# Kernel tuning notes

Hardware: AMD Instinct MI355X
Metric: run time of the kernel (lower is better)

The kernel has to match this reference:

```python
import jax, jax.numpy as jnp
import numpy as np

B, D_IN, D_Z, D_H, D_T, D_REC = 8192, 1024, 256, 256, 16, 256


def _softplus_beta(x, beta):
    # torch F.softplus(x, beta) = (1/beta) * log(1 + exp(beta*x))
    return jax.nn.softplus(beta * x) / beta


def setup_inputs() -> dict:
    key = jax.random.key(0)
    ks = jax.random.split(key, 17)
    w = lambda k, o, i: jax.random.normal(k, (o, i), jnp.float32) * (1.0 / np.sqrt(i))
    return {
        "I_t": jax.random.uniform(ks[0], (B, D_IN), jnp.float32),
        "h_m_1": jax.random.uniform(ks[1], (B, D_H), jnp.float32),
        "z_m_1": jax.random.uniform(ks[2], (B, D_Z), jnp.float32),
        "theta_m_1": jax.random.normal(ks[3], (B, D_T), jnp.float32),
        "eps_z": jax.random.normal(ks[4], (B, D_Z), jnp.float32),
        "eps_zhat": jax.random.normal(ks[5], (B, D_Z), jnp.float32),
        "W_post_mu": w(ks[6], D_Z, D_IN),
        "W_post_lv": w(ks[7], D_Z, D_IN),
        "W_z2h": w(ks[8], D_H, D_Z),
        "W_h2h": w(ks[9], D_H, D_H),
        "W_prior_mu": w(ks[10], D_Z, D_H),
        "W_prior_lv": w(ks[11], D_Z, D_H),
        "W_i2t": w(ks[12], D_T, D_IN),
        "W_vip2t": w(ks[13], D_T, D_Z),
        "W_t2z": w(ks[14], D_Z, D_T),
        "W_rec1": w(ks[15], D_REC, D_Z),
        "W_rec2": w(ks[16], D_IN, D_REC),
    }


def reference(I_t, h_m_1, z_m_1, theta_m_1, eps_z, eps_zhat,
              W_post_mu, W_post_lv, W_z2h, W_h2h, W_prior_mu, W_prior_lv,
              W_i2t, W_vip2t, W_t2z, W_rec1, W_rec2):
    relu = jax.nn.relu
    # prior pathway (perception_only=True branch)
    mu_p = relu(h_m_1 @ W_prior_mu.T)                       # [B, D_Z]
    sigma_p = _softplus_beta(h_m_1 @ W_prior_lv.T, 1.2)     # [B, D_Z]
    # theta dynamics; vip_to_theta has Positive parametrization -> relu(W)
    theta_h = (0.5 * theta_m_1 + 0.1 * (I_t @ W_i2t.T)
               - jax.lax.stop_gradient(sigma_p) @ relu(W_vip2t).T)  # [B, D_T]
    theta = 0.001 * _softplus_beta(theta_h, 0.5)
    # posterior + reparameterized sample
    mu_q = relu(I_t @ W_post_mu.T)
    sigma_q = relu(I_t @ W_post_lv.T)
    raw_z = jnp.clip(mu_q + eps_z * sigma_q, 0.0, 1.0)
    thresholds = 10.0 * (theta @ relu(W_t2z).T)             # Positive parametrization
    z = relu(raw_z - thresholds)                            # [B, D_Z]
    # reconstruction (two bias-free linears + sigmoid)
    I_hat = jax.nn.sigmoid((z @ W_rec1.T) @ W_rec2.T)       # [B, D_IN]
    # higher-state update and prior sample
    h = relu(z_m_1 @ W_z2h.T + h_m_1 @ W_h2h.T)             # [B, D_H]
    z_hat = mu_p + eps_zhat * sigma_p                       # [B, D_Z]
    # losses (as in torch forward)
    spatial = jnp.mean((I_t - I_hat) ** 2)
    temporal = jnp.mean((jax.lax.stop_gradient(z) - z_hat) ** 2)
    energy = jnp.mean(jnp.abs(z))
    return (I_hat, z, h, z_hat, spatial, temporal, energy)
```

## Files before the change

kernel.cpp:

```cpp
#include <hip/hip_runtime.h>
#include <math.h>

#define BB 8192
#define DIN 1024
#define DZ 256
#define DH 256
#define DT 16
#define DREC 256

#define OFF_IHAT 0
#define OFF_Z    (BB * DIN)
#define OFF_H    (OFF_Z + BB * DZ)
#define OFF_ZHAT (OFF_H + BB * DH)
#define OFF_SCAL (OFF_ZHAT + BB * DZ)

#define WS_HBF   0
#define WS_ZM1   2097152
#define WS_W     4194304
#define W_PM  (WS_W + 0)
#define W_PL  (W_PM + 262144)
#define W_Z2H (W_PL + 262144)
#define W_H2H (W_Z2H + 65536)
#define W_PRM (W_H2H + 65536)
#define W_PRL (W_PRM + 65536)
#define W_I2T (W_PRL + 65536)
#define W_VIP (W_I2T + 16384)
#define W_R1  (W_VIP + 4096)
#define W_R2  (W_R1 + 65536)
#define WS_ENDW  (W_R2 + 262144)
#define WS_SIGMA WS_ENDW
#define WS_ZBF   (WS_SIGMA + 2097152)
#define WS_R1BF  (WS_ZBF + 2097152)

typedef unsigned short u16;
typedef __attribute__((ext_vector_type(8))) unsigned short u16x8;
typedef __attribute__((ext_vector_type(8))) __bf16 bf16x8;
typedef __attribute__((ext_vector_type(4))) float f32x4;

#define MFMA __builtin_amdgcn_mfma_f32_16x16x32_bf16

__device__ inline u16 f2bf(float f) {
  unsigned u = __builtin_bit_cast(unsigned, f);
  u += 0x7fff + ((u >> 16) & 1);
  return (u16)(u >> 16);
}
__device__ inline float softplus_stable(float y) {
  return (y > 20.f) ? y : log1pf(expf(y));
}
__device__ inline bf16x8 gf(const u16* p) {
  return __builtin_bit_cast(bf16x8, *(const u16x8*)p);
}
__device__ inline f32x4 fzero() { return (f32x4){0.f, 0.f, 0.f, 0.f}; }

__device__ inline float block_sum256(float v, float* rbuf) {
#pragma unroll
  for (int off = 32; off > 0; off >>= 1) v += __shfl_down(v, off, 64);
  __syncthreads();
  if ((threadIdx.x & 63) == 0) rbuf[threadIdx.x >> 6] = v;
  __syncthreads();
  return rbuf[0] + rbuf[1] + rbuf[2] + rbuf[3];
}
__device__ inline float block_sum512(float v, float* rbuf) {
#pragma unroll
  for (int off = 32; off > 0; off >>= 1) v += __shfl_down(v, off, 64);
  __syncthreads();
  if ((threadIdx.x & 63) == 0) rbuf[threadIdx.x >> 6] = v;
  __syncthreads();
  float s = 0.f;
#pragma unroll
  for (int i = 0; i < 8; ++i) s += rbuf[i];
  return s;
}

__device__ inline void decode4(int id, int rows, int& row0, int& col0) {
  int xcd = id & 7, t = id >> 3;
  col0 = (t & 3) * 64;
  row0 = ((t >> 2) * 8 + xcd) * rows;
}

__device__ inline void dmaA32(u16* tile, const u16* __restrict__ gsrc,
                              int row0, int ldk, int k0) {
  const int lane = threadIdx.x & 63, w = threadIdx.x >> 6;
  int rb = w * 8;
  int r = rb + (lane >> 3);
  int gl = (lane & 7) ^ (r & 7);
  const u16* src = gsrc + (size_t)(row0 + r) * ldk + k0 + gl * 8;
  u16* dst = tile + rb * 64;
  __builtin_amdgcn_global_load_lds(
      (const __attribute__((address_space(1))) unsigned int*)(const void*)src,
      (__attribute__((address_space(3))) unsigned int*)(void*)dst, 16, 0, 0);
}
__device__ inline void dmaB64(u16* tile, const u16* __restrict__ gsrc,
                              int row0, int ldk, int k0) {
  const int lane = threadIdx.x & 63, w = threadIdx.x >> 6;
#pragma unroll
  for (int c = 0; c < 2; ++c) {
    int rb = w * 16 + c * 8;
    int r = rb + (lane >> 3);
    int gl = (lane & 7) ^ (r & 7);
    const u16* src = gsrc + (size_t)(row0 + r) * ldk + k0 + gl * 8;
    u16* dst = tile + rb * 64;
    __builtin_amdgcn_global_load_lds(
        (const __attribute__((address_space(1))) unsigned int*)(const void*)src,
        (__attribute__((address_space(3))) unsigned int*)(void*)dst, 16, 0, 0);
  }
}
__device__ inline bf16x8 rd(const u16* tile, int r, int gl) {
  return gf(tile + r * 64 + ((gl ^ (r & 7)) * 8));
}

__device__ inline void stg64x256(u16* tile, const u16* __restrict__ g,
                                 int row0, int ldk, int k0) {
  const int lane = threadIdx.x & 63, w = threadIdx.x >> 6;
#pragma unroll
  for (int i = 0; i < 4; ++i) {
    int rb = (w * 4 + i) * 2;
    int r = rb + (lane >> 5);
    int d = lane & 31;
    int s = d ^ (r & 7);
    const u16* src = g + (size_t)(row0 + r) * ldk + k0 + s * 8;
    u16* dst = tile + rb * 256;
    __builtin_amdgcn_global_load_lds(
        (const __attribute__((address_space(1))) unsigned int*)(const void*)src,
        (__attribute__((address_space(3))) unsigned int*)(void*)dst, 16, 0, 0);
  }
}
__device__ inline void stg16x256(u16* tile, const u16* __restrict__ g,
                                 int ldk, int k0) {
  const int lane = threadIdx.x & 63, w = threadIdx.x >> 6;
  int rb = w * 2;
  int r = rb + (lane >> 5);
  int d = lane & 31;
  int s = d ^ (r & 7);
  const u16* src = g + (size_t)r * ldk + k0 + s * 8;
  u16* dst = tile + rb * 256;
  __builtin_amdgcn_global_load_lds(
      (const __attribute__((address_space(1))) unsigned int*)(const void*)src,
      (__attribute__((address_space(3))) unsigned int*)(void*)dst, 16, 0, 0);
}
__device__ inline bf16x8 rd256(const u16* tile, int r, int j) {
  return gf(tile + r * 256 + ((j ^ (r & 7)) * 8));
}

__global__ __launch_bounds__(256) void k_cvt(
    const float* __restrict__ I_t, const float* __restrict__ h_m_1,
    const float* __restrict__ z_m_1, const float* __restrict__ Wpm,
    const float* __restrict__ Wpl, const float* __restrict__ Wz2h,
    const float* __restrict__ Wh2h, const float* __restrict__ Wprm,
    const float* __restrict__ Wprl, const float* __restrict__ Wi2t,
    const float* __restrict__ Wv, const float* __restrict__ Wr1,
    const float* __restrict__ Wr2, u16* __restrict__ dstI,
    u16* __restrict__ dstW) {
  const int S1 = 8388608, S2 = 10485760, S3 = 12582912, S4 = 12845056,
            S5 = 13107200, S6 = 13172736, S7 = 13238272, S8 = 13303808,
            S9 = 13369344, S10 = 13385728, S11 = 13389824, S12 = 13455360,
            S13 = 13717504;
  int nchunk = S13 / 8;
  for (int c = blockIdx.x * 256 + threadIdx.x; c < nchunk;
       c += gridDim.x * 256) {
    int f = c * 8;
    const float* src;
    float scale = 1.f;
    bool nrelu = false;
    u16* dst;
    if (f < S1) {
      src = I_t + f;
      dst = dstI + f;
    } else {
      dst = dstW + (f - S1);
      if (f < S2)       src = h_m_1 + (f - S1);
      else if (f < S3)  src = z_m_1 + (f - S2);
      else if (f < S4)  src = Wpm + (f - S3);
      else if (f < S5)  src = Wpl + (f - S4);
      else if (f < S6)  src = Wz2h + (f - S5);
      else if (f < S7)  src = Wh2h + (f - S6);
      else if (f < S8)  src = Wprm + (f - S7);
      else if (f < S9)  src = Wprl + (f - S8);
      else if (f < S10) { src = Wi2t + (f - S9);  scale = 0.1f; }
      else if (f < S11) { src = Wv + (f - S10);   nrelu = true; }
      else if (f < S12) src = Wr1 + (f - S11);
      else              src = Wr2 + (f - S12);
    }
    float4 v0 = *(const float4*)(src);
    float4 v1 = *(const float4*)(src + 4);
    float vals[8] = {v0.x, v0.y, v0.z, v0.w, v1.x, v1.y, v1.z, v1.w};
    u16x8 o;
#pragma unroll
    for (int j = 0; j < 8; ++j) {
      float x = vals[j];
      x = nrelu ? -fmaxf(x, 0.f) : x * scale;
      o[j] = f2bf(x);
    }
    *(u16x8*)(dst) = o;
  }
}

__global__ __launch_bounds__(256, 4) void k_hp(
    const u16* __restrict__ h_bf, const u16* __restrict__ zm1,
    const u16* __restrict__ Wh2h, const u16* __restrict__ Wprm,
    const u16* __restrict__ Wprl, const u16* __restrict__ Wz2h,
    const float* __restrict__ eps_zhat, float* __restrict__ h_out,
    float* __restrict__ zhat_out, u16* __restrict__ sigma_bf) {
  __shared__ __align__(16) u16 smem[2048 + 3 * 4096];
  u16* As = smem;
  u16* B0s = smem + 2048;
  u16* B1s = B0s + 4096;
  u16* B2s = B1s + 4096;
  const int tid = threadIdx.x, lane = tid & 63, w = tid >> 6;
  const int frow = lane & 15, fq = lane >> 4;
  const int wr = w & 1, wc = w >> 1;
  int row0, col0;
  decode4(blockIdx.x, 32, row0, col0);

  f32x4 ah[2], am[2], as_[2];
#pragma unroll
  for (int i = 0; i < 2; ++i) { ah[i] = fzero(); am[i] = fzero(); as_[i] = fzero(); }

  for (int k0 = 0; k0 < DH; k0 += 64) {
    __syncthreads();
    dmaA32(As, h_bf, row0, DH, k0);
    dmaB64(B0s, Wh2h, col0, DH, k0);
    dmaB64(B1s, Wprm, col0, DH, k0);
    dmaB64(B2s, Wprl, col0, DH, k0);
    __syncthreads();
#pragma unroll
    for (int ks = 0; ks < 2; ++ks) {
      bf16x8 a = rd(As, wr * 16 + frow, ks * 4 + fq);
#pragma unroll
      for (int ni = 0; ni < 2; ++ni) {
        int br = wc * 32 + ni * 16 + frow;
        ah[ni]  = MFMA(a, rd(B0s, br, ks * 4 + fq), ah[ni], 0, 0, 0);
        am[ni]  = MFMA(a, rd(B1s, br, ks * 4 + fq), am[ni], 0, 0, 0);
        as_[ni] = MFMA(a, rd(B2s, br, ks * 4 + fq), as_[ni], 0, 0, 0);
      }
    }
  }
  for (int k0 = 0; k0 < DZ; k0 += 64) {
    __syncthreads();
    dmaA32(As, zm1, row0, DZ, k0);
    dmaB64(B0s, Wz2h, col0, DZ, k0);
    __syncthreads();
#pragma unroll
    for (int ks = 0; ks < 2; ++ks) {
      bf16x8 a = rd(As, wr * 16 + frow, ks * 4 + fq);
#pragma unroll
      for (int ni = 0; ni < 2; ++ni)
        ah[ni] = MFMA(a, rd(B0s, wc * 32 + ni * 16 + frow, ks * 4 + fq),
                      ah[ni], 0, 0, 0);
    }
  }
  __syncthreads();
  float* ht = (float*)smem;
  float* mt = (float*)(smem + 4224);
  float* st = (float*)(smem + 8448);
#pragma unroll
  for (int ni = 0; ni < 2; ++ni)
#pragma unroll
    for (int r = 0; r < 4; ++r) {
      int lr = wr * 16 + fq * 4 + r;
      int ln = wc * 32 + ni * 16 + frow;
      ht[lr * 66 + ln] = fmaxf(ah[ni][r], 0.f);
      mt[lr * 66 + ln] = fmaxf(am[ni][r], 0.f);
      st[lr * 66 + ln] = softplus_stable(1.2f * as_[ni][r]) * (1.f / 1.2f);
    }
  __syncthreads();
  {
    int lr2 = tid >> 3, c0 = (tid & 7) * 8;
    int m2 = row0 + lr2;
    float h8[8], mu8[8], sg8[8];
#pragma unroll
    for (int j = 0; j < 8; ++j) {
      h8[j] = ht[lr2 * 66 + c0 + j];
      mu8[j] = mt[lr2 * 66 + c0 + j];
      sg8[j] = st[lr2 * 66 + c0 + j];
    }
    float* hp = h_out + (size_t)m2 * DH + col0 + c0;
    *(float4*)hp = make_float4(h8[0], h8[1], h8[2], h8[3]);
    *(float4*)(hp + 4) = make_float4(h8[4], h8[5], h8[6], h8[7]);
    const float* ep = eps_zhat + (size_t)m2 * DZ + col0 + c0;
    float4 e0 = ((const float4*)ep)[0], e1 = ((const float4*)ep)[1];
    float e8[8] = {e0.x, e0.y, e0.z, e0.w, e1.x, e1.y, e1.z, e1.w};
    float zh8[8];
    u16x8 sb;
#pragma unroll
    for (int j = 0; j < 8; ++j) {
      zh8[j] = mu8[j] + e8[j] * sg8[j];
      sb[j] = f2bf(sg8[j]);
    }
    float* zp = zhat_out + (size_t)m2 * DZ + col0 + c0;
    *(float4*)zp = make_float4(zh8[0], zh8[1], zh8[2], zh8[3]);
    *(float4*)(zp + 4) = make_float4(zh8[4], zh8[5], zh8[6], zh8[7]);
    *(u16x8*)(sigma_bf + (size_t)m2 * DZ + col0 + c0) = sb;
  }
}

__global__ __launch_bounds__(512, 2) void k_post(
    const u16* __restrict__ I_bf, const u16* __restrict__ Wpm,
    const u16* __restrict__ Wpl, const u16* __restrict__ Wi2t,
    const u16* __restrict__ Wv, const u16* __restrict__ sigma_bf,
    const float* __restrict__ theta_m_1, const float* __restrict__ W_t2z,
    const float* __restrict__ eps_z, const float* __restrict__ zhat,
    float* __restrict__ z_out, u16* __restrict__ z_bf,
    float* __restrict__ scal) {
  __shared__ __align__(16) u16 smem[36864];
  __shared__ float thwt[128 * 17 + 64 * 17];
  __shared__ float rbuf[8];
  const int tid = threadIdx.x, lane = tid & 63, w = tid >> 6;
  const int frow = lane & 15, fq = lane >> 4;
  int row0, col0;
  {
    int xcd = blockIdx.x & 7, t = blockIdx.x >> 3;
    col0 = (t & 3) * 64;
    row0 = ((t >> 2) * 8 + xcd) * 128;
  }
  u16* b0 = smem;

  f32x4 mu[4], sg[4], tt = fzero();
#pragma unroll
  for (int i = 0; i < 4; ++i) { mu[i] = fzero(); sg[i] = fzero(); }

  const u16* Abase = I_bf + (size_t)(row0 + w * 16 + frow) * DIN;
  const u16* Sbase = sigma_bf + (size_t)(row0 + w * 16 + frow) * DZ;
  bf16x8 ar[8];

#pragma unroll 1
  for (int p = 0; p < 4; ++p) {
    int kwin = p * 256;
    stg64x256(b0, Wpm, col0, DIN, kwin);
    stg64x256(b0 + 16384, Wpl, col0, DIN, kwin);
    stg16x256(b0 + 32768, Wi2t, DIN, kwin);
#pragma unroll
    for (int kk = 0; kk < 8; ++kk)
      ar[kk] = gf(Abase + kwin + kk * 32 + fq * 8);
    __syncthreads();
#pragma unroll
    for (int kk = 0; kk < 8; ++kk) {
#pragma unroll
      for (int n = 0; n < 4; ++n) {
        mu[n] = MFMA(ar[kk], rd256(b0, n * 16 + frow, kk * 4 + fq),
                     mu[n], 0, 0, 0);
        sg[n] = MFMA(ar[kk], rd256(b0 + 16384, n * 16 + frow, kk * 4 + fq),
                     sg[n], 0, 0, 0);
      }
      tt = MFMA(ar[kk], rd256(b0 + 32768, frow, kk * 4 + fq), tt, 0, 0, 0);
    }
    __syncthreads();
  }
  stg16x256(b0 + 32768, Wv, DZ, 0);
#pragma unroll
  for (int kk = 0; kk < 8; ++kk) ar[kk] = gf(Sbase + kk * 32 + fq * 8);
  __syncthreads();
#pragma unroll
  for (int kk = 0; kk < 8; ++kk)
    tt = MFMA(ar[kk], rd256(b0 + 32768, frow, kk * 4 + fq), tt, 0, 0, 0);
  __syncthreads();

  float* mt   = (float*)smem;
  float* st   = (float*)(smem + 16896);
  float* th_s = thwt;
  float* wt_s = thwt + 128 * 17;

#pragma unroll
  for (int r = 0; r < 4; ++r) {
    int lr = w * 16 + fq * 4 + r;
    float th = 0.5f * theta_m_1[(size_t)(row0 + lr) * DT + frow] + tt[r];
    th_s[lr * 17 + frow] = 0.002f * softplus_stable(0.5f * th);
  }
  for (int idx = tid; idx < 64 * 16; idx += 512) {
    int n = idx >> 4, j = idx & 15;
    wt_s[n * 17 + j] = 10.f * fmaxf(W_t2z[(col0 + n) * DT + j], 0.f);
  }
#pragma unroll
  for (int n = 0; n < 4; ++n)
#pragma unroll
    for (int r = 0; r < 4; ++r) {
      int lr = w * 16 + fq * 4 + r;
      int ln = n * 16 + frow;
      mt[lr * 66 + ln] = fmaxf(mu[n][r], 0.f);
      st[lr * 66 + ln] = fmaxf(sg[n][r], 0.f);
    }
  __syncthreads();
  float tsum = 0.f, esum = 0.f;
  {
    int lr2 = tid >> 2, c0 = (tid & 3) * 16;
    int m2 = row0 + lr2;
    float thv[16];
#pragma unroll
    for (int j = 0; j < 16; ++j) thv[j] = th_s[lr2 * 17 + j];
#pragma unroll
    for (int gb = 0; gb < 2; ++gb) {
      int c = c0 + gb * 8;
      float mu8[8], sg8[8];
#pragma unroll
      for (int j = 0; j < 8; ++j) {
        mu8[j] = mt[lr2 * 66 + c + j];
        sg8[j] = st[lr2 * 66 + c + j];
      }
      const float* ep = eps_z + (size_t)m2 * DZ + col0 + c;
      float4 e0 = ((const float4*)ep)[0], e1 = ((const float4*)ep)[1];
      float e8[8] = {e0.x, e0.y, e0.z, e0.w, e1.x, e1.y, e1.z, e1.w};
      float z8[8];
#pragma unroll
      for (int j = 0; j < 8; ++j) {
        float raw = mu8[j] + e8[j] * sg8[j];
        raw = fminf(fmaxf(raw, 0.f), 1.f);
        float thr = 0.f;
#pragma unroll
        for (int jj = 0; jj < 16; ++jj)
          thr = fmaf(thv[jj], wt_s[(c + j) * 17 + jj], thr);
        z8[j] = fmaxf(raw - thr, 0.f);
      }
      float* zp = z_out + (size_t)m2 * DZ + col0 + c;
      *(float4*)zp = make_float4(z8[0], z8[1], z8[2], z8[3]);
      *(float4*)(zp + 4) = make_float4(z8[4], z8[5], z8[6], z8[7]);
      u16x8 zb;
#pragma unroll
      for (int j = 0; j < 8; ++j) zb[j] = f2bf(z8[j]);
      *(u16x8*)(z_bf + (size_t)m2 * DZ + col0 + c) = zb;
      const float* zhp = zhat + (size_t)m2 * DZ + col0 + c;
      float4 h0 = ((const float4*)zhp)[0], h1 = ((const float4*)zhp)[1];
      float zh8[8] = {h0.x, h0.y, h0.z, h0.w, h1.x, h1.y, h1.z, h1.w};
#pragma unroll
      for (int j = 0; j < 8; ++j) {
        float d = z8[j] - zh8[j];
        tsum += d * d;
        esum += z8[j];
      }
    }
  }
  float t = block_sum512(tsum, rbuf);
  if (tid == 0) atomicAdd(scal + 1, t * (1.f / ((float)BB * DZ)));
  float e = block_sum512(esum, rbuf);
  if (tid == 0) atomicAdd(scal + 2, e * (1.f / ((float)BB * DZ)));
}

__global__ __launch_bounds__(256, 4) void k_rec1(const u16* __restrict__ z_bf,
                                                 const u16* __restrict__ Wr1,
                                                 u16* __restrict__ r1_bf) {
  __shared__ __align__(16) u16 smem[2048 + 4096];
  u16* As = smem;
  u16* B0s = smem + 2048;
  const int tid = threadIdx.x, lane = tid & 63, w = tid >> 6;
  const int frow = lane & 15, fq = lane >> 4;
  const int wr = w & 1, wc = w >> 1;
  int row0, col0;
  decode4(blockIdx.x, 32, row0, col0);
  f32x4 acc[2] = {fzero(), fzero()};
  for (int k0 = 0; k0 < DZ; k0 += 64) {
    __syncthreads();
    dmaA32(As, z_bf, row0, DZ, k0);
    dmaB64(B0s, Wr1, col0, DZ, k0);
    __syncthreads();
#pragma unroll
    for (int ks = 0; ks < 2; ++ks) {
      bf16x8 a = rd(As, wr * 16 + frow, ks * 4 + fq);
#pragma unroll
      for (int ni = 0; ni < 2; ++ni)
        acc[ni] = MFMA(a, rd(B0s, wc * 32 + ni * 16 + frow, ks * 4 + fq),
                       acc[ni], 0, 0, 0);
    }
  }
  __syncthreads();
  float* rt = (float*)smem;
#pragma unroll
  for (int ni = 0; ni < 2; ++ni)
#pragma unroll
    for (int r = 0; r < 4; ++r) {
      int lr = wr * 16 + fq * 4 + r;
      int ln = wc * 32 + ni * 16 + frow;
      rt[lr * 66 + ln] = acc[ni][r];
    }
  __syncthreads();
  {
    int lr2 = tid >> 3, c0 = (tid & 7) * 8;
    int m2 = row0 + lr2;
    u16x8 rb;
#pragma unroll
    for (int j = 0; j < 8; ++j) rb[j] = f2bf(rt[lr2 * 66 + c0 + j]);
    *(u16x8*)(r1_bf + (size_t)m2 * DREC + col0 + c0) = rb;
  }
}

__global__ __launch_bounds__(256, 4) void k_rec2(const u16* __restrict__ r1_bf,
                                                 const u16* __restrict__ Wr2,
                                                 const float* __restrict__ I_t,
                                                 float* __restrict__ ihat_out,
                                                 float* __restrict__ scal) {
  __shared__ __align__(16) u16 smem[4096 + 4096];
  u16* As = smem;
  u16* B0s = smem + 4096;
  __shared__ float rbuf[4];
  const int tid = threadIdx.x, lane = tid & 63, w = tid >> 6;
  const int frow = lane & 15, fq = lane >> 4;
  int row0, col0;
  {
    int id = blockIdx.x;
    int xcd = id & 7, t = id >> 3;
    col0 = (t & 15) * 64;
    row0 = ((t >> 4) * 8 + xcd) * 64;
  }
  f32x4 acc[4] = {fzero(), fzero(), fzero(), fzero()};
  for (int k0 = 0; k0 < DREC; k0 += 64) {
    __syncthreads();
    dmaB64(As, r1_bf, row0, DREC, k0);
    dmaB64(B0s, Wr2, col0, DREC, k0);
    __syncthreads();
#pragma unroll
    for (int ks = 0; ks < 2; ++ks) {
      bf16x8 a = rd(As, w * 16 + frow, ks * 4 + fq);
#pragma unroll
      for (int ni = 0; ni < 4; ++ni)
        acc[ni] = MFMA(a, rd(B0s, ni * 16 + frow, ks * 4 + fq), acc[ni], 0, 0, 0);
    }
  }
  float lsum = 0.f;
  float* it = (float*)smem;
#pragma unroll 1
  for (int p = 0; p < 2; ++p) {
    __syncthreads();
    if ((w >> 1) == p) {
#pragma unroll
      for (int ni = 0; ni < 4; ++ni)
#pragma unroll
        for (int r = 0; r < 4; ++r) {
          int lrl = (w & 1) * 16 + fq * 4 + r;
          int ln = ni * 16 + frow;
          it[lrl * 66 + ln] = 1.f / (1.f + expf(-acc[ni][r]));
        }
    }
    __syncthreads();
    int lr2 = tid >> 3, c0 = (tid & 7) * 8;
    int m2 = row0 + p * 32 + lr2;
    float i8[8];
#pragma unroll
    for (int j = 0; j < 8; ++j) i8[j] = it[lr2 * 66 + c0 + j];
    float* op = ihat_out + (size_t)m2 * DIN + col0 + c0;
    *(float4*)op = make_float4(i8[0], i8[1], i8[2], i8[3]);
    *(float4*)(op + 4) = make_float4(i8[4], i8[5], i8[6], i8[7]);
    const float* ip = I_t + (size_t)m2 * DIN + col0 + c0;
    float4 a0 = ((const float4*)ip)[0], a1 = ((const float4*)ip)[1];
    float t8[8] = {a0.x, a0.y, a0.z, a0.w, a1.x, a1.y, a1.z, a1.w};
#pragma unroll
    for (int j = 0; j < 8; ++j) {
      float d = t8[j] - i8[j];
      lsum += d * d;
    }
  }
  float s = block_sum256(lsum, rbuf);
  if (tid == 0) atomicAdd(scal + 0, s * (1.f / ((float)BB * DIN)));
}

extern "C" void kernel_launch(void* const* d_in, const int* in_sizes, int n_in,
                              void* d_out, int out_size, void* d_ws,
                              size_t ws_size, hipStream_t stream) {
  const float* I_t       = (const float*)d_in[0];
  const float* h_m_1     = (const float*)d_in[1];
  const float* z_m_1     = (const float*)d_in[2];
  const float* theta_m_1 = (const float*)d_in[3];
  const float* eps_z     = (const float*)d_in[4];
  const float* eps_zhat  = (const float*)d_in[5];
  const float* W_post_mu = (const float*)d_in[6];
  const float* W_post_lv = (const float*)d_in[7];
  const float* W_z2h     = (const float*)d_in[8];
  const float* W_h2h     = (const float*)d_in[9];
  const float* W_prior_mu= (const float*)d_in[10];
  const float* W_prior_lv= (const float*)d_in[11];
  const float* W_i2t     = (const float*)d_in[12];
  const float* W_vip2t   = (const float*)d_in[13];
  const float* W_t2z     = (const float*)d_in[14];
  const float* W_rec1    = (const float*)d_in[15];
  const float* W_rec2    = (const float*)d_in[16];

  float* out = (float*)d_out;
  float* ihat = out + OFF_IHAT;
  float* zout = out + OFF_Z;
  float* hout = out + OFF_H;
  float* zhat = out + OFF_ZHAT;
  float* scal = out + OFF_SCAL;

  u16* ws_u = (u16*)d_ws;
  u16* I_bf = (u16*)ihat;
  u16* h_bf = ws_u + WS_HBF;
  u16* zm1_bf = ws_u + WS_ZM1;
  u16* sigma_bf = ws_u + WS_SIGMA;
  u16* z_bf = ws_u + WS_ZBF;
  u16* r1_bf = ws_u + WS_R1BF;

  hipMemsetAsync(scal, 0, 3 * sizeof(float), stream);

  k_cvt<<<2048, 256, 0, stream>>>(I_t, h_m_1, z_m_1, W_post_mu, W_post_lv,
                                  W_z2h, W_h2h, W_prior_mu, W_prior_lv, W_i2t,
                                  W_vip2t, W_rec1, W_rec2, I_bf, ws_u + WS_HBF);

  k_hp<<<1024, 256, 0, stream>>>(h_bf, zm1_bf, ws_u + W_H2H, ws_u + W_PRM,
                                 ws_u + W_PRL, ws_u + W_Z2H, eps_zhat, hout,
                                 zhat, sigma_bf);
  k_post<<<256, 512, 0, stream>>>(I_bf, ws_u + W_PM, ws_u + W_PL,
                                  ws_u + W_I2T, ws_u + W_VIP, sigma_bf,
                                  theta_m_1, W_t2z, eps_z, zhat, zout, z_bf,
                                  scal);
  k_rec1<<<1024, 256, 0, stream>>>(z_bf, ws_u + W_R1, r1_bf);
  k_rec2<<<2048, 256, 0, stream>>>(r1_bf, ws_u + W_R2, I_t, ihat, scal);
}
```

Baseline: 238.3 us.

## Double-buffer LDS staging in hp, post, rec1 and rec2 GEMM kernels

Converts the K-loops of the four GEMM kernels to double-buffered shared memory. The next K slice is issued with global_load_lds while the current slice is consumed, so each step needs one barrier instead of two. The posterior kernel drops from 256-wide K windows to 128-wide windows across two alternating buffers, prefetching A fragments into alternating register sets in a fully unrolled sequence. The point is to overlap global-to-LDS transfer with MFMA work. The cost is twice the LDS per block, a lower occupancy hint for k_hp (4 to 2 blocks), and more registers for the prefetched A fragments.

```diff
diff --git a/kernel.cpp b/kernel.cpp
--- a/kernel.cpp
+++ b/kernel.cpp
@@ -109,37 +109,64 @@
   return gf(tile + r * 64 + ((gl ^ (r & 7)) * 8));
 }
 
-__device__ inline void stg64x256(u16* tile, const u16* __restrict__ g,
+__device__ inline void stg64x128(u16* tile, const u16* __restrict__ g,
                                  int row0, int ldk, int k0) {
   const int lane = threadIdx.x & 63, w = threadIdx.x >> 6;
 #pragma unroll
-  for (int i = 0; i < 4; ++i) {
-    int rb = (w * 4 + i) * 2;
-    int r = rb + (lane >> 5);
-    int d = lane & 31;
+  for (int i = 0; i < 2; ++i) {
+    int rb = (w * 2 + i) * 4;
+    int r = rb + (lane >> 4);
+    int d = lane & 15;
     int s = d ^ (r & 7);
     const u16* src = g + (size_t)(row0 + r) * ldk + k0 + s * 8;
-    u16* dst = tile + rb * 256;
+    u16* dst = tile + rb * 128;
     __builtin_amdgcn_global_load_lds(
         (const __attribute__((address_space(1))) unsigned int*)(const void*)src,
         (__attribute__((address_space(3))) unsigned int*)(void*)dst, 16, 0, 0);
   }
 }
-__device__ inline void stg16x256(u16* tile, const u16* __restrict__ g,
+__device__ inline void stg16x128(u16* tile, const u16* __restrict__ g,
                                  int ldk, int k0) {
   const int lane = threadIdx.x & 63, w = threadIdx.x >> 6;
-  int rb = w * 2;
-  int r = rb + (lane >> 5);
-  int d = lane & 31;
-  int s = d ^ (r & 7);
-  const u16* src = g + (size_t)r * ldk + k0 + s * 8;
-  u16* dst = tile + rb * 256;
-  __builtin_amdgcn_global_load_lds(
-      (const __attribute__((address_space(1))) unsigned int*)(const void*)src,
-      (__attribute__((address_space(3))) unsigned int*)(void*)dst, 16, 0, 0);
-}
-__device__ inline bf16x8 rd256(const u16* tile, int r, int j) {
-  return gf(tile + r * 256 + ((j ^ (r & 7)) * 8));
+  if (w < 4) {
+    int rb = w * 4;
+    int r = rb + (lane >> 4);
+    int d = lane & 15;
+    int s = d ^ (r & 7);
+    const u16* src = g + (size_t)r * ldk + k0 + s * 8;
+    u16* dst = tile + rb * 128;
+    __builtin_amdgcn_global_load_lds(
+        (const __attribute__((address_space(1))) unsigned int*)(const void*)src,
+        (__attribute__((address_space(3))) unsigned int*)(void*)dst, 16, 0, 0);
+  }
+}
+__device__ inline bf16x8 rd128(const u16* tile, int r, int j) {
+  return gf(tile + r * 128 + ((j ^ (r & 7)) * 8));
+}
+
+__device__ inline void lda4(bf16x8 (&ar)[4], const u16* base, int kwin,
+                            int fq) {
+#pragma unroll
+  for (int kk = 0; kk < 4; ++kk) ar[kk] = gf(base + kwin + kk * 32 + fq * 8);
+}
+__device__ inline void cmpMain(const u16* buf, bf16x8 (&ar)[4], f32x4 (&mu)[4],
+                               f32x4 (&sg)[4], f32x4& tt, int frow, int fq) {
+#pragma unroll
+  for (int kk = 0; kk < 4; ++kk) {
+    int j = kk * 4 + fq;
+#pragma unroll
+    for (int n = 0; n < 4; ++n) {
+      mu[n] = MFMA(ar[kk], rd128(buf, n * 16 + frow, j), mu[n], 0, 0, 0);
+      sg[n] = MFMA(ar[kk], rd128(buf + 8192, n * 16 + frow, j), sg[n], 0, 0, 0);
+    }
+    tt = MFMA(ar[kk], rd128(buf + 16384, frow, j), tt, 0, 0, 0);
+  }
+}
+__device__ inline void cmpSig(const u16* buf, bf16x8 (&ar)[4], f32x4& tt,
+                              int frow, int fq) {
+#pragma unroll
+  for (int kk = 0; kk < 4; ++kk)
+    tt = MFMA(ar[kk], rd128(buf + 16384, frow, kk * 4 + fq), tt, 0, 0, 0);
 }
 
 __global__ __launch_bounds__(256) void k_cvt(
@@ -195,17 +222,13 @@
   }
 }
 
-__global__ __launch_bounds__(256, 4) void k_hp(
+__global__ __launch_bounds__(256, 2) void k_hp(
     const u16* __restrict__ h_bf, const u16* __restrict__ zm1,
     const u16* __restrict__ Wh2h, const u16* __restrict__ Wprm,
     const u16* __restrict__ Wprl, const u16* __restrict__ Wz2h,
     const float* __restrict__ eps_zhat, float* __restrict__ h_out,
     float* __restrict__ zhat_out, u16* __restrict__ sigma_bf) {
-  __shared__ __align__(16) u16 smem[2048 + 3 * 4096];
-  u16* As = smem;
-  u16* B0s = smem + 2048;
-  u16* B1s = B0s + 4096;
-  u16* B2s = B1s + 4096;
+  __shared__ __align__(16) u16 smem[2 * 14336];
   const int tid = threadIdx.x, lane = tid & 63, w = tid >> 6;
   const int frow = lane & 15, fq = lane >> 4;
   const int wr = w & 1, wc = w >> 1;
@@ -216,37 +239,55 @@
 #pragma unroll
   for (int i = 0; i < 2; ++i) { ah[i] = fzero(); am[i] = fzero(); as_[i] = fzero(); }
 
-  for (int k0 = 0; k0 < DH; k0 += 64) {
+  dmaA32(smem, h_bf, row0, DH, 0);
+  dmaB64(smem + 2048, Wh2h, col0, DH, 0);
+  dmaB64(smem + 6144, Wprm, col0, DH, 0);
+  dmaB64(smem + 10240, Wprl, col0, DH, 0);
+
+#pragma unroll 1
+  for (int t = 0; t < 8; ++t) {
     __syncthreads();
-    dmaA32(As, h_bf, row0, DH, k0);
-    dmaB64(B0s, Wh2h, col0, DH, k0);
-    dmaB64(B1s, Wprm, col0, DH, k0);
-    dmaB64(B2s, Wprl, col0, DH, k0);
-    __syncthreads();
-#pragma unroll
-    for (int ks = 0; ks < 2; ++ks) {
-      bf16x8 a = rd(As, wr * 16 + frow, ks * 4 + fq);
-#pragma unroll
-      for (int ni = 0; ni < 2; ++ni) {
-        int br = wc * 32 + ni * 16 + frow;
-        ah[ni]  = MFMA(a, rd(B0s, br, ks * 4 + fq), ah[ni], 0, 0, 0);
-        am[ni]  = MFMA(a, rd(B1s, br, ks * 4 + fq), am[ni], 0, 0, 0);
-        as_[ni] = MFMA(a, rd(B2s, br, ks * 4 + fq), as_[ni], 0, 0, 0);
+    u16* cs = smem + (t & 1) * 14336;
+    u16* ns = smem + ((t + 1) & 1) * 14336;
+    if (t < 7) {
+      int u = t + 1;
+      if (u < 4) {
+        int k0 = u * 64;
+        dmaA32(ns, h_bf, row0, DH, k0);
+        dmaB64(ns + 2048, Wh2h, col0, DH, k0);
+        dmaB64(ns + 6144, Wprm, col0, DH, k0);
+        dmaB64(ns + 10240, Wprl, col0, DH, k0);
+      } else {
+        int k0 = (u - 4) * 64;
+        dmaA32(ns, zm1, row0, DZ, k0);
+        dmaB64(ns + 2048, Wz2h, col0, DZ, k0);
       }
     }
-  }
-  for (int k0 = 0; k0 < DZ; k0 += 64) {
-    __syncthreads();
-    dmaA32(As, zm1, row0, DZ, k0);
-    dmaB64(B0s, Wz2h, col0, DZ, k0);
-    __syncthreads();
-#pragma unroll
-    for (int ks = 0; ks < 2; ++ks) {
-      bf16x8 a = rd(As, wr * 16 + frow, ks * 4 + fq);
-#pragma unroll
-      for (int ni = 0; ni < 2; ++ni)
-        ah[ni] = MFMA(a, rd(B0s, wc * 32 + ni * 16 + frow, ks * 4 + fq),
-                      ah[ni], 0, 0, 0);
+    const u16* As = cs;
+    const u16* B0s = cs + 2048;
+    if (t < 4) {
+      const u16* B1s = cs + 6144;
+      const u16* B2s = cs + 10240;
+#pragma unroll
+      for (int ks = 0; ks < 2; ++ks) {
+        bf16x8 a = rd(As, wr * 16 + frow, ks * 4 + fq);
+#pragma unroll
+        for (int ni = 0; ni < 2; ++ni) {
+          int br = wc * 32 + ni * 16 + frow;
+          ah[ni]  = MFMA(a, rd(B0s, br, ks * 4 + fq), ah[ni], 0, 0, 0);
+          am[ni]  = MFMA(a, rd(B1s, br, ks * 4 + fq), am[ni], 0, 0, 0);
+          as_[ni] = MFMA(a, rd(B2s, br, ks * 4 + fq), as_[ni], 0, 0, 0);
+        }
+      }
+    } else {
+#pragma unroll
+      for (int ks = 0; ks < 2; ++ks) {
+        bf16x8 a = rd(As, wr * 16 + frow, ks * 4 + fq);
+#pragma unroll
+        for (int ni = 0; ni < 2; ++ni)
+          ah[ni] = MFMA(a, rd(B0s, wc * 32 + ni * 16 + frow, ks * 4 + fq),
+                        ah[ni], 0, 0, 0);
+      }
     }
   }
   __syncthreads();
@@ -302,7 +343,7 @@
     const float* __restrict__ eps_z, const float* __restrict__ zhat,
     float* __restrict__ z_out, u16* __restrict__ z_bf,
     float* __restrict__ scal) {
-  __shared__ __align__(16) u16 smem[36864];
+  __shared__ __align__(16) u16 smem[2 * 18432];
   __shared__ float thwt[128 * 17 + 64 * 17];
   __shared__ float rbuf[8];
   const int tid = threadIdx.x, lane = tid & 63, w = tid >> 6;
@@ -314,6 +355,7 @@
     row0 = ((t >> 2) * 8 + xcd) * 128;
   }
   u16* b0 = smem;
+  u16* b1 = smem + 18432;
 
   f32x4 mu[4], sg[4], tt = fzero();
 #pragma unroll
@@ -321,40 +363,38 @@
 
   const u16* Abase = I_bf + (size_t)(row0 + w * 16 + frow) * DIN;
   const u16* Sbase = sigma_bf + (size_t)(row0 + w * 16 + frow) * DZ;
-  bf16x8 ar[8];
-
-#pragma unroll 1
-  for (int p = 0; p < 4; ++p) {
-    int kwin = p * 256;
-    stg64x256(b0, Wpm, col0, DIN, kwin);
-    stg64x256(b0 + 16384, Wpl, col0, DIN, kwin);
-    stg16x256(b0 + 32768, Wi2t, DIN, kwin);
-#pragma unroll
-    for (int kk = 0; kk < 8; ++kk)
-      ar[kk] = gf(Abase + kwin + kk * 32 + fq * 8);
-    __syncthreads();
-#pragma unroll
-    for (int kk = 0; kk < 8; ++kk) {
-#pragma unroll
-      for (int n = 0; n < 4; ++n) {
-        mu[n] = MFMA(ar[kk], rd256(b0, n * 16 + frow, kk * 4 + fq),
-                     mu[n], 0, 0, 0);
-        sg[n] = MFMA(ar[kk], rd256(b0 + 16384, n * 16 + frow, kk * 4 + fq),
-                     sg[n], 0, 0, 0);
-      }
-      tt = MFMA(ar[kk], rd256(b0 + 32768, frow, kk * 4 + fq), tt, 0, 0, 0);
-    }
-    __syncthreads();
-  }
-  stg16x256(b0 + 32768, Wv, DZ, 0);
-#pragma unroll
-  for (int kk = 0; kk < 8; ++kk) ar[kk] = gf(Sbase + kk * 32 + fq * 8);
-  __syncthreads();
-#pragma unroll
-  for (int kk = 0; kk < 8; ++kk)
-    tt = MFMA(ar[kk], rd256(b0 + 32768, frow, kk * 4 + fq), tt, 0, 0, 0);
-  __syncthreads();
-
+  bf16x8 arA[4], arB[4];
+
+#define STGM(buf, k0)                        \
+  stg64x128(buf, Wpm, col0, DIN, k0);        \
+  stg64x128((buf) + 8192, Wpl, col0, DIN, k0);\
+  stg16x128((buf) + 16384, Wi2t, DIN, k0)
+
+  STGM(b0, 0);
+  lda4(arA, Abase, 0, fq);
+  __syncthreads(); STGM(b1, 128); lda4(arB, Abase, 128, fq);
+  cmpMain(b0, arA, mu, sg, tt, frow, fq);
+  __syncthreads(); STGM(b0, 256); lda4(arA, Abase, 256, fq);
+  cmpMain(b1, arB, mu, sg, tt, frow, fq);
+  __syncthreads(); STGM(b1, 384); lda4(arB, Abase, 384, fq);
+  cmpMain(b0, arA, mu, sg, tt, frow, fq);
+  __syncthreads(); STGM(b0, 512); lda4(arA, Abase, 512, fq);
+  cmpMain(b1, arB, mu, sg, tt, frow, fq);
+  __syncthreads(); STGM(b1, 640); lda4(arB, Abase, 640, fq);
+  cmpMain(b0, arA, mu, sg, tt, frow, fq);
+  __syncthreads(); STGM(b0, 768); lda4(arA, Abase, 768, fq);
+  cmpMain(b1, arB, mu, sg, tt, frow, fq);
+  __syncthreads(); STGM(b1, 896); lda4(arB, Abase, 896, fq);
+  cmpMain(b0, arA, mu, sg, tt, frow, fq);
+  __syncthreads(); stg16x128(b0 + 16384, Wv, DZ, 0); lda4(arA, Sbase, 0, fq);
+  cmpMain(b1, arB, mu, sg, tt, frow, fq);
+  __syncthreads(); stg16x128(b1 + 16384, Wv, DZ, 128); lda4(arB, Sbase, 128, fq);
+  cmpSig(b0, arA, tt, frow, fq);
+  __syncthreads();
+  cmpSig(b1, arB, tt, frow, fq);
+#undef STGM
+
+  __syncthreads();
   float* mt   = (float*)smem;
   float* st   = (float*)(smem + 16896);
   float* th_s = thwt;
@@ -437,26 +477,32 @@
 __global__ __launch_bounds__(256, 4) void k_rec1(const u16* __restrict__ z_bf,
                                                  const u16* __restrict__ Wr1,
                                                  u16* __restrict__ r1_bf) {
-  __shared__ __align__(16) u16 smem[2048 + 4096];
-  u16* As = smem;
-  u16* B0s = smem + 2048;
+  __shared__ __align__(16) u16 smem[2 * 6144];
   const int tid = threadIdx.x, lane = tid & 63, w = tid >> 6;
   const int frow = lane & 15, fq = lane >> 4;
   const int wr = w & 1, wc = w >> 1;
   int row0, col0;
   decode4(blockIdx.x, 32, row0, col0);
   f32x4 acc[2] = {fzero(), fzero()};
-  for (int k0 = 0; k0 < DZ; k0 += 64) {
+
+  dmaA32(smem, z_bf, row0, DZ, 0);
+  dmaB64(smem + 2048, Wr1, col0, DZ, 0);
+#pragma unroll 1
+  for (int t = 0; t < 4; ++t) {
     __syncthreads();
-    dmaA32(As, z_bf, row0, DZ, k0);
-    dmaB64(B0s, Wr1, col0, DZ, k0);
-    __syncthreads();
+    u16* cs = smem + (t & 1) * 6144;
+    u16* ns = smem + ((t + 1) & 1) * 6144;
+    if (t < 3) {
+      int k0 = (t + 1) * 64;
+      dmaA32(ns, z_bf, row0, DZ, k0);
+      dmaB64(ns + 2048, Wr1, col0, DZ, k0);
+    }
 #pragma unroll
     for (int ks = 0; ks < 2; ++ks) {
-      bf16x8 a = rd(As, wr * 16 + frow, ks * 4 + fq);
+      bf16x8 a = rd(cs, wr * 16 + frow, ks * 4 + fq);
 #pragma unroll
       for (int ni = 0; ni < 2; ++ni)
-        acc[ni] = MFMA(a, rd(B0s, wc * 32 + ni * 16 + frow, ks * 4 + fq),
+        acc[ni] = MFMA(a, rd(cs + 2048, wc * 32 + ni * 16 + frow, ks * 4 + fq),
                        acc[ni], 0, 0, 0);
     }
   }
@@ -486,9 +532,7 @@
                                                  const float* __restrict__ I_t,
                                                  float* __restrict__ ihat_out,
                                                  float* __restrict__ scal) {
-  __shared__ __align__(16) u16 smem[4096 + 4096];
-  u16* As = smem;
-  u16* B0s = smem + 4096;
+  __shared__ __align__(16) u16 smem[2 * 8192];
   __shared__ float rbuf[4];
   const int tid = threadIdx.x, lane = tid & 63, w = tid >> 6;
   const int frow = lane & 15, fq = lane >> 4;
@@ -500,17 +544,26 @@
     row0 = ((t >> 4) * 8 + xcd) * 64;
   }
   f32x4 acc[4] = {fzero(), fzero(), fzero(), fzero()};
-  for (int k0 = 0; k0 < DREC; k0 += 64) {
+
+  dmaB64(smem, r1_bf, row0, DREC, 0);
+  dmaB64(smem + 4096, Wr2, col0, DREC, 0);
+#pragma unroll 1
+  for (int t = 0; t < 4; ++t) {
     __syncthreads();
-    dmaB64(As, r1_bf, row0, DREC, k0);
-    dmaB64(B0s, Wr2, col0, DREC, k0);
-    __syncthreads();
+    u16* cs = smem + (t & 1) * 8192;
+    u16* ns = smem + ((t + 1) & 1) * 8192;
+    if (t < 3) {
+      int k0 = (t + 1) * 64;
+      dmaB64(ns, r1_bf, row0, DREC, k0);
+      dmaB64(ns + 4096, Wr2, col0, DREC, k0);
+    }
 #pragma unroll
     for (int ks = 0; ks < 2; ++ks) {
-      bf16x8 a = rd(As, w * 16 + frow, ks * 4 + fq);
+      bf16x8 a = rd(cs, w * 16 + frow, ks * 4 + fq);
 #pragma unroll
       for (int ni = 0; ni < 4; ++ni)
-        acc[ni] = MFMA(a, rd(B0s, ni * 16 + frow, ks * 4 + fq), acc[ni], 0, 0, 0);
+        acc[ni] = MFMA(a, rd(cs + 4096, ni * 16 + frow, ks * 4 + fq),
+                       acc[ni], 0, 0, 0);
     }
   }
   float lsum = 0.f;
```

New measurement: 236.3 us. Within noise of the previous version (-0.8%).

## Double-buffer k_post weight staging and give each wave two row tiles

Applied to the files above, without the earlier changes.

Rewrites the posterior kernel to use 256 threads, with each wave handling 32 rows (two MFMA row tiles) so every LDS B-fragment read is reused twice. K windows shrink to 128 and alternate between two LDS buffers, so the next window's global-to-LDS DMA and A-register loads overlap MFMA work on the current one. The aim is to hide load latency and cut LDS read traffic. In exchange, register pressure per thread doubles and fewer waves are resident, since launch bounds drop to 256 threads with min 1 block.

```diff
diff --git a/kernel.cpp b/kernel.cpp
--- a/kernel.cpp
+++ b/kernel.cpp
@@ -60,17 +60,6 @@
   __syncthreads();
   return rbuf[0] + rbuf[1] + rbuf[2] + rbuf[3];
 }
-__device__ inline float block_sum512(float v, float* rbuf) {
-#pragma unroll
-  for (int off = 32; off > 0; off >>= 1) v += __shfl_down(v, off, 64);
-  __syncthreads();
-  if ((threadIdx.x & 63) == 0) rbuf[threadIdx.x >> 6] = v;
-  __syncthreads();
-  float s = 0.f;
-#pragma unroll
-  for (int i = 0; i < 8; ++i) s += rbuf[i];
-  return s;
-}
 
 __device__ inline void decode4(int id, int rows, int& row0, int& col0) {
   int xcd = id & 7, t = id >> 3;
@@ -109,37 +98,75 @@
   return gf(tile + r * 64 + ((gl ^ (r & 7)) * 8));
 }
 
-__device__ inline void stg64x256(u16* tile, const u16* __restrict__ g,
-                                 int row0, int ldk, int k0) {
+__device__ inline void stg64q(u16* tile, const u16* __restrict__ g,
+                              int row0, int ldk, int k0) {
   const int lane = threadIdx.x & 63, w = threadIdx.x >> 6;
 #pragma unroll
   for (int i = 0; i < 4; ++i) {
-    int rb = (w * 4 + i) * 2;
-    int r = rb + (lane >> 5);
-    int d = lane & 31;
+    int rb = w * 16 + i * 4;
+    int r = rb + (lane >> 4);
+    int d = lane & 15;
     int s = d ^ (r & 7);
     const u16* src = g + (size_t)(row0 + r) * ldk + k0 + s * 8;
-    u16* dst = tile + rb * 256;
+    u16* dst = tile + rb * 128;
     __builtin_amdgcn_global_load_lds(
         (const __attribute__((address_space(1))) unsigned int*)(const void*)src,
         (__attribute__((address_space(3))) unsigned int*)(void*)dst, 16, 0, 0);
   }
 }
-__device__ inline void stg16x256(u16* tile, const u16* __restrict__ g,
-                                 int ldk, int k0) {
+__device__ inline void stg16q(u16* tile, const u16* __restrict__ g,
+                              int ldk, int k0) {
   const int lane = threadIdx.x & 63, w = threadIdx.x >> 6;
-  int rb = w * 2;
-  int r = rb + (lane >> 5);
-  int d = lane & 31;
+  int rb = w * 4;
+  int r = rb + (lane >> 4);
+  int d = lane & 15;
   int s = d ^ (r & 7);
   const u16* src = g + (size_t)r * ldk + k0 + s * 8;
-  u16* dst = tile + rb * 256;
+  u16* dst = tile + rb * 128;
   __builtin_amdgcn_global_load_lds(
       (const __attribute__((address_space(1))) unsigned int*)(const void*)src,
       (__attribute__((address_space(3))) unsigned int*)(void*)dst, 16, 0, 0);
 }
-__device__ inline bf16x8 rd256(const u16* tile, int r, int j) {
-  return gf(tile + r * 256 + ((j ^ (r & 7)) * 8));
+__device__ inline bf16x8 rd128(const u16* tile, int r, int j) {
+  return gf(tile + r * 128 + ((j ^ (r & 7)) * 8));
+}
+
+__device__ inline void lda8(bf16x8 (&ar)[2][4], const u16* a0, const u16* a1,
+                            int kwin, int fq) {
+#pragma unroll
+  for (int kk = 0; kk < 4; ++kk) {
+    ar[0][kk] = gf(a0 + kwin + kk * 32 + fq * 8);
+    ar[1][kk] = gf(a1 + kwin + kk * 32 + fq * 8);
+  }
+}
+__device__ inline void cmpMain2(const u16* buf, bf16x8 (&ar)[2][4],
+                                f32x4 (&mu)[2][4], f32x4 (&sg)[2][4],
+                                f32x4 (&tt)[2], int frow, int fq) {
+#pragma unroll
+  for (int kk = 0; kk < 4; ++kk) {
+    int j = kk * 4 + fq;
+#pragma unroll
+    for (int n = 0; n < 4; ++n) {
+      bf16x8 bm = rd128(buf, n * 16 + frow, j);
+      mu[0][n] = MFMA(ar[0][kk], bm, mu[0][n], 0, 0, 0);
+      mu[1][n] = MFMA(ar[1][kk], bm, mu[1][n], 0, 0, 0);
+      bf16x8 bs = rd128(buf + 8192, n * 16 + frow, j);
+      sg[0][n] = MFMA(ar[0][kk], bs, sg[0][n], 0, 0, 0);
+      sg[1][n] = MFMA(ar[1][kk], bs, sg[1][n], 0, 0, 0);
+    }
+    bf16x8 bt = rd128(buf + 16384, frow, j);
+    tt[0] = MFMA(ar[0][kk], bt, tt[0], 0, 0, 0);
+    tt[1] = MFMA(ar[1][kk], bt, tt[1], 0, 0, 0);
+  }
+}
+__device__ inline void cmpSig2(const u16* buf, bf16x8 (&ar)[2][4],
+                               f32x4 (&tt)[2], int frow, int fq) {
+#pragma unroll
+  for (int kk = 0; kk < 4; ++kk) {
+    bf16x8 bt = rd128(buf + 16384, frow, kk * 4 + fq);
+    tt[0] = MFMA(ar[0][kk], bt, tt[0], 0, 0, 0);
+    tt[1] = MFMA(ar[1][kk], bt, tt[1], 0, 0, 0);
+  }
 }
 
 __global__ __launch_bounds__(256) void k_cvt(
@@ -294,7 +321,7 @@
   }
 }
 
-__global__ __launch_bounds__(512, 2) void k_post(
+__global__ __launch_bounds__(256, 1) void k_post(
     const u16* __restrict__ I_bf, const u16* __restrict__ Wpm,
     const u16* __restrict__ Wpl, const u16* __restrict__ Wi2t,
     const u16* __restrict__ Wv, const u16* __restrict__ sigma_bf,
@@ -302,9 +329,9 @@
     const float* __restrict__ eps_z, const float* __restrict__ zhat,
     float* __restrict__ z_out, u16* __restrict__ z_bf,
     float* __restrict__ scal) {
-  __shared__ __align__(16) u16 smem[36864];
+  __shared__ __align__(16) u16 smem[2 * 18432];
   __shared__ float thwt[128 * 17 + 64 * 17];
-  __shared__ float rbuf[8];
+  __shared__ float rbuf[4];
   const int tid = threadIdx.x, lane = tid & 63, w = tid >> 6;
   const int frow = lane & 15, fq = lane >> 4;
   int row0, col0;
@@ -314,81 +341,91 @@
     row0 = ((t >> 2) * 8 + xcd) * 128;
   }
   u16* b0 = smem;
-
-  f32x4 mu[4], sg[4], tt = fzero();
-#pragma unroll
-  for (int i = 0; i < 4; ++i) { mu[i] = fzero(); sg[i] = fzero(); }
-
-  const u16* Abase = I_bf + (size_t)(row0 + w * 16 + frow) * DIN;
-  const u16* Sbase = sigma_bf + (size_t)(row0 + w * 16 + frow) * DZ;
-  bf16x8 ar[8];
-
-#pragma unroll 1
-  for (int p = 0; p < 4; ++p) {
-    int kwin = p * 256;
-    stg64x256(b0, Wpm, col0, DIN, kwin);
-    stg64x256(b0 + 16384, Wpl, col0, DIN, kwin);
-    stg16x256(b0 + 32768, Wi2t, DIN, kwin);
-#pragma unroll
-    for (int kk = 0; kk < 8; ++kk)
-      ar[kk] = gf(Abase + kwin + kk * 32 + fq * 8);
-    __syncthreads();
-#pragma unroll
-    for (int kk = 0; kk < 8; ++kk) {
-#pragma unroll
-      for (int n = 0; n < 4; ++n) {
-        mu[n] = MFMA(ar[kk], rd256(b0, n * 16 + frow, kk * 4 + fq),
-                     mu[n], 0, 0, 0);
-        sg[n] = MFMA(ar[kk], rd256(b0 + 16384, n * 16 + frow, kk * 4 + fq),
-                     sg[n], 0, 0, 0);
-      }
-      tt = MFMA(ar[kk], rd256(b0 + 32768, frow, kk * 4 + fq), tt, 0, 0, 0);
-    }
-    __syncthreads();
-  }
-  stg16x256(b0 + 32768, Wv, DZ, 0);
-#pragma unroll
-  for (int kk = 0; kk < 8; ++kk) ar[kk] = gf(Sbase + kk * 32 + fq * 8);
-  __syncthreads();
-#pragma unroll
-  for (int kk = 0; kk < 8; ++kk)
-    tt = MFMA(ar[kk], rd256(b0 + 32768, frow, kk * 4 + fq), tt, 0, 0, 0);
-  __syncthreads();
-
+  u16* b1 = smem + 18432;
+
+  f32x4 mu[2][4], sg[2][4], tt[2];
+#pragma unroll
+  for (int m = 0; m < 2; ++m) {
+    tt[m] = fzero();
+#pragma unroll
+    for (int n = 0; n < 4; ++n) { mu[m][n] = fzero(); sg[m][n] = fzero(); }
+  }
+
+  const u16* Ai0 = I_bf + (size_t)(row0 + w * 32 + frow) * DIN;
+  const u16* Ai1 = Ai0 + (size_t)16 * DIN;
+  const u16* As0 = sigma_bf + (size_t)(row0 + w * 32 + frow) * DZ;
+  const u16* As1 = As0 + (size_t)16 * DZ;
+  bf16x8 arA[2][4], arB[2][4];
+
+#define STGM(buf, k0)                       \
+  stg64q(buf, Wpm, col0, DIN, k0);          \
+  stg64q((buf) + 8192, Wpl, col0, DIN, k0); \
+  stg16q((buf) + 16384, Wi2t, DIN, k0)
+
+  STGM(b0, 0);
+  lda8(arA, Ai0, Ai1, 0, fq);
+  __syncthreads(); STGM(b1, 128); lda8(arB, Ai0, Ai1, 128, fq);
+  cmpMain2(b0, arA, mu, sg, tt, frow, fq);
+  __syncthreads(); STGM(b0, 256); lda8(arA, Ai0, Ai1, 256, fq);
+  cmpMain2(b1, arB, mu, sg, tt, frow, fq);
+  __syncthreads(); STGM(b1, 384); lda8(arB, Ai0, Ai1, 384, fq);
+  cmpMain2(b0, arA, mu, sg, tt, frow, fq);
+  __syncthreads(); STGM(b0, 512); lda8(arA, Ai0, Ai1, 512, fq);
+  cmpMain2(b1, arB, mu, sg, tt, frow, fq);
+  __syncthreads(); STGM(b1, 640); lda8(arB, Ai0, Ai1, 640, fq);
+  cmpMain2(b0, arA, mu, sg, tt, frow, fq);
+  __syncthreads(); STGM(b0, 768); lda8(arA, Ai0, Ai1, 768, fq);
+  cmpMain2(b1, arB, mu, sg, tt, frow, fq);
+  __syncthreads(); STGM(b1, 896); lda8(arB, Ai0, Ai1, 896, fq);
+  cmpMain2(b0, arA, mu, sg, tt, frow, fq);
+  __syncthreads(); stg16q(b0 + 16384, Wv, DZ, 0); lda8(arA, As0, As1, 0, fq);
+  cmpMain2(b1, arB, mu, sg, tt, frow, fq);
+  __syncthreads(); stg16q(b1 + 16384, Wv, DZ, 128);
+  lda8(arB, As0, As1, 128, fq);
+  cmpSig2(b0, arA, tt, frow, fq);
+  __syncthreads();
+  cmpSig2(b1, arB, tt, frow, fq);
+#undef STGM
+
+  __syncthreads();
   float* mt   = (float*)smem;
   float* st   = (float*)(smem + 16896);
   float* th_s = thwt;
   float* wt_s = thwt + 128 * 17;
 
 #pragma unroll
-  for (int r = 0; r < 4; ++r) {
-    int lr = w * 16 + fq * 4 + r;
-    float th = 0.5f * theta_m_1[(size_t)(row0 + lr) * DT + frow] + tt[r];
-    th_s[lr * 17 + frow] = 0.002f * softplus_stable(0.5f * th);
-  }
-  for (int idx = tid; idx < 64 * 16; idx += 512) {
+  for (int m = 0; m < 2; ++m)
+#pragma unroll
+    for (int r = 0; r < 4; ++r) {
+      int lr = w * 32 + m * 16 + fq * 4 + r;
+      float th = 0.5f * theta_m_1[(size_t)(row0 + lr) * DT + frow] + tt[m][r];
+      th_s[lr * 17 + frow] = 0.002f * softplus_stable(0.5f * th);
+    }
+  for (int idx = tid; idx < 64 * 16; idx += 256) {
     int n = idx >> 4, j = idx & 15;
     wt_s[n * 17 + j] = 10.f * fmaxf(W_t2z[(col0 + n) * DT + j], 0.f);
   }
 #pragma unroll
-  for (int n = 0; n < 4; ++n)
-#pragma unroll
-    for (int r = 0; r < 4; ++r) {
-      int lr = w * 16 + fq * 4 + r;
-      int ln = n * 16 + frow;
-      mt[lr * 66 + ln] = fmaxf(mu[n][r], 0.f);
-      st[lr * 66 + ln] = fmaxf(sg[n][r], 0.f);
-    }
+  for (int m = 0; m < 2; ++m)
+#pragma unroll
+    for (int n = 0; n < 4; ++n)
+#pragma unroll
+      for (int r = 0; r < 4; ++r) {
+        int lr = w * 32 + m * 16 + fq * 4 + r;
+        int ln = n * 16 + frow;
+        mt[lr * 66 + ln] = fmaxf(mu[m][n][r], 0.f);
+        st[lr * 66 + ln] = fmaxf(sg[m][n][r], 0.f);
+      }
   __syncthreads();
   float tsum = 0.f, esum = 0.f;
   {
-    int lr2 = tid >> 2, c0 = (tid & 3) * 16;
+    int lr2 = tid >> 1, c0 = (tid & 1) * 32;
     int m2 = row0 + lr2;
     float thv[16];
 #pragma unroll
     for (int j = 0; j < 16; ++j) thv[j] = th_s[lr2 * 17 + j];
 #pragma unroll
-    for (int gb = 0; gb < 2; ++gb) {
+    for (int gb = 0; gb < 4; ++gb) {
       int c = c0 + gb * 8;
       float mu8[8], sg8[8];
 #pragma unroll
@@ -428,9 +465,9 @@
       }
     }
   }
-  float t = block_sum512(tsum, rbuf);
+  float t = block_sum256(tsum, rbuf);
   if (tid == 0) atomicAdd(scal + 1, t * (1.f / ((float)BB * DZ)));
-  float e = block_sum512(esum, rbuf);
+  float e = block_sum256(esum, rbuf);
   if (tid == 0) atomicAdd(scal + 2, e * (1.f / ((float)BB * DZ)));
 }
 
@@ -595,7 +632,7 @@
   k_hp<<<1024, 256, 0, stream>>>(h_bf, zm1_bf, ws_u + W_H2H, ws_u + W_PRM,
                                  ws_u + W_PRL, ws_u + W_Z2H, eps_zhat, hout,
                                  zhat, sigma_bf);
-  k_post<<<256, 512, 0, stream>>>(I_bf, ws_u + W_PM, ws_u + W_PL,
+  k_post<<<256, 256, 0, stream>>>(I_bf, ws_u + W_PM, ws_u + W_PL,
                                   ws_u + W_I2T, ws_u + W_VIP, sigma_bf,
                                   theta_m_1, W_t2z, eps_z, zhat, zout, z_bf,
                                   scal);
```

New measurement: 241.3 us. About the same (+1.2%).
